# Kernel tuning notes

Measured on AMD Instinct MI355X. Metric: run time of the kernel, lower is better.

Reference implementation:

```python
import jax, jax.numpy as jnp
import numpy as np

N, R, C_IN, C_OUT, MODES = 8, 256, 64, 64, 16


def setup_inputs() -> dict:
    key = jax.random.key(0)
    k1, k2, k3, k4, k5 = jax.random.split(key, 5)
    # xavier-like scale used in the torch init: gain/(in*out)*sqrt(in+out) folded into std
    std = (1.0 / (C_IN * C_OUT)) * np.sqrt(2.0)  # small, keeps spectra sane
    return {
        "X": jax.random.normal(k1, (N, R, R, C_IN), dtype=jnp.float32),
        "W_res": jax.random.normal(k2, (C_IN, C_OUT), dtype=jnp.float32) / np.sqrt(C_IN),
        "b_res": jax.random.normal(k3, (C_OUT,), dtype=jnp.float32) * 0.01,
        "fw0": jax.random.normal(k4, (C_IN, C_OUT, MODES, MODES, 2), dtype=jnp.float32) * std,
        "fw1": jax.random.normal(k5, (C_IN, C_OUT, MODES, MODES, 2), dtype=jnp.float32) * std,
    }


def reference(X, W_res, b_res, fw0, fw1):
    # X: [N, r, r, in_dim]
    n, r, _, _ = X.shape
    modes = fw0.shape[2]
    out_dim = fw0.shape[1]

    res = X @ W_res + b_res  # [N, r, r, out_dim]  (dropout p=0.0 -> identity)

    Xc = jnp.transpose(X, (0, 3, 1, 2))  # [N, in, r, r]
    X_ft = jnp.fft.rfft2(Xc, s=(r, r), norm="ortho")  # [N, in, r, r//2+1] complex

    w0 = fw0[..., 0] + 1j * fw0[..., 1]  # [in, out, m, m] complex
    w1 = fw1[..., 0] + 1j * fw1[..., 1]

    top = jnp.einsum("bixy,ioxy->boxy", X_ft[:, :, :modes, :modes], w0)
    bot = jnp.einsum("bixy,ioxy->boxy", X_ft[:, :, r - modes :, :modes], w1)

    out_ft = jnp.zeros((n, out_dim, r, r // 2 + 1), dtype=X_ft.dtype)
    out_ft = out_ft.at[:, :, :modes, :modes].set(top)
    out_ft = out_ft.at[:, :, r - modes :, :modes].set(bot)

    Xo = jnp.fft.irfft2(out_ft, s=(r, r), norm="ortho")  # [N, out, r, r] real
    Xo = jnp.transpose(Xo, (0, 2, 3, 1))  # [N, r, r, out]
    return jax.nn.silu(Xo + res)
```

## Files before the change

kernel.cpp:

```cpp
#include <hip/hip_runtime.h>
#include <math.h>

#define RDIM 256
#define CIN 64
#define COUT 64
#define MODES 16
#define NB 8

typedef short short8 __attribute__((ext_vector_type(8)));
typedef float f32x4 __attribute__((ext_vector_type(4)));

__device__ __forceinline__ unsigned short f2b(float f) {
    unsigned u = __builtin_bit_cast(unsigned, f);
    unsigned r = (u + 0x7FFFu + ((u >> 16) & 1u)) >> 16;
    return (unsigned short)r;
}

__device__ __forceinline__ void build_tab(float2* tab) {
    for (int p = (int)threadIdx.x; p < 256; p += (int)blockDim.x) {
        float ang = (float)p * (float)(2.0 * M_PI / 256.0);
        float s, c;
        sincosf(ang, &s, &c);
        tab[p] = make_float2(c, s);
    }
}

__global__ __launch_bounds__(256) void k_tf(unsigned short* __restrict__ Tf) {
    int e = blockIdx.x * 256 + (int)threadIdx.x;
    int kyc = e >> 8, y = e & 255, ky = kyc >> 1;
    int p = (ky * y) & 255;
    float ang = (float)p * (float)(2.0 * M_PI / 256.0);
    float s, c;
    sincosf(ang, &s, &c);
    Tf[e] = f2b((kyc & 1) ? -s : c);
}

__global__ __launch_bounds__(256) void k_wt(const float* __restrict__ fw0,
                                            const float* __restrict__ fw1,
                                            float2* __restrict__ WT) {
    __shared__ float2 Ls[16][257];
    int blk = blockIdx.x;
    int arr = blk >> 8;
    int tile = blk & 255;
    const float2* s2 = (const float2*)(arr ? fw1 : fw0);
    int t = (int)threadIdx.x;
    for (int e = t; e < 4096; e += 256) {
        int oo = e >> 8;
        int q = e & 255;
        Ls[oo][q] = s2[(size_t)(tile * 16 + oo) * 256 + q];
    }
    __syncthreads();
    int i = (tile * 16) >> 6;
    int o0 = (tile * 16) & 63;
    for (int e = t; e < 4096; e += 256) {
        int oo = e & 15;
        int q = e >> 4;
        int mx = q >> 4, ky = q & 15;
        int m = arr * 16 + mx;
        WT[((size_t)(m * 16 + ky) * 64 + i) * 64 + o0 + oo] = Ls[oo][q];
    }
}

__global__ __launch_bounds__(256) void k_prep(const float* __restrict__ Wres,
                                              unsigned short* __restrict__ WbT,
                                              unsigned short* __restrict__ Tg) {
    int e = blockIdx.x * 256 + (int)threadIdx.x;
    if (e < 4096) {
        int o = e >> 6, k = e & 63;
        WbT[o * 64 + k] = f2b(Wres[k * 64 + o]);
    } else {
        int f = e - 4096;
        int y = f >> 5, kk = f & 31, ky = kk >> 1;
        int p = (ky * y) & 255;
        float ang = (float)p * (float)(2.0 * M_PI / 256.0);
        float s, c;
        sincosf(ang, &s, &c);
        Tg[f] = f2b((kk & 1) ? -s : c);
    }
}

__global__ __launch_bounds__(256) void k_fwd_y(const float* __restrict__ X,
                                               const unsigned short* __restrict__ Tf,
                                               float2* __restrict__ A) {
    __shared__ short8 Xb[64 * 32];
    int b = blockIdx.x >> 8;
    int x = blockIdx.x & 255;
    int t = (int)threadIdx.x;
    int w = t >> 6;
    int l = t & 63;

    const float* Xr = X + ((size_t)(b * 256 + x)) * 256 * 64;
#pragma unroll
    for (int s = 0; s < 8; s++) {
        int y8 = w * 8 + s;
        const float* base = Xr + (size_t)y8 * 512 + l;
        short8 hb;
#pragma unroll
        for (int j = 0; j < 8; j++) hb[j] = (short)f2b(base[j * 64]);
        Xb[l * 32 + (y8 ^ (l & 7))] = hb;
    }
    __syncthreads();

    int m16 = l & 15;
    int quad = l >> 4;
    int iRow = w * 16 + m16;
    int isw = iRow & 7;

    f32x4 acc0 = (f32x4){0.f, 0.f, 0.f, 0.f};
    f32x4 acc1 = (f32x4){0.f, 0.f, 0.f, 0.f};
    const unsigned short* T0 = Tf + (size_t)m16 * 256 + quad * 8;
#pragma unroll
    for (int ks = 0; ks < 8; ks++) {
        short8 a0 = *(const short8*)(T0 + ks * 32);
        short8 a1 = *(const short8*)(T0 + 4096 + ks * 32);
        int y8r = ks * 4 + quad;
        short8 bfrag = Xb[iRow * 32 + (y8r ^ isw)];
        acc0 = __builtin_amdgcn_mfma_f32_16x16x32_bf16(a0, bfrag, acc0, 0, 0, 0);
        acc1 = __builtin_amdgcn_mfma_f32_16x16x32_bf16(a1, bfrag, acc1, 0, 0, 0);
    }

    float2* Aout = A + ((size_t)(b * 256 + x)) * 16 * 64;
    int ky0 = (quad * 4) >> 1;
    Aout[(size_t)ky0 * 64 + iRow] = make_float2(acc0[0], acc0[1]);
    Aout[(size_t)(ky0 + 1) * 64 + iRow] = make_float2(acc0[2], acc0[3]);
    int ky1 = (16 + quad * 4) >> 1;
    Aout[(size_t)ky1 * 64 + iRow] = make_float2(acc1[0], acc1[1]);
    Aout[(size_t)(ky1 + 1) * 64 + iRow] = make_float2(acc1[2], acc1[3]);
}

__global__ __launch_bounds__(256) void k_fwd_x(const float2* __restrict__ A,
                                               float2* __restrict__ C) {
    __shared__ float2 tab[256];
    __shared__ float2 red[4 * 8 * 64];
    int bi = blockIdx.x;
    int b = bi >> 6;
    int ky = (bi >> 2) & 15;
    int mg = bi & 3;
    build_tab(tab);
    __syncthreads();
    int t = (int)threadIdx.x;
    int i = t & 63;
    int xg = t >> 6;
    float cr[8], ci[8];
    int pj[8], st[8];
#pragma unroll
    for (int j = 0; j < 8; j++) {
        cr[j] = 0.f; ci[j] = 0.f;
        int m = mg * 8 + j;
        int kx = (m < 16) ? m : (m + 224);
        pj[j] = (kx * xg) & 255;
        st[j] = (kx * 4) & 255;
    }
    const float2* Ap = A + ((size_t)b * 256) * 16 * 64 + ky * 64 + i;
    for (int x = xg; x < 256; x += 4) {
        float2 a = Ap[(size_t)x * 16 * 64];
#pragma unroll
        for (int j = 0; j < 8; j++) {
            float2 tc = tab[pj[j]];
            pj[j] = (pj[j] + st[j]) & 255;
            cr[j] += a.x * tc.x + a.y * tc.y;
            ci[j] += a.y * tc.x - a.x * tc.y;
        }
    }
#pragma unroll
    for (int j = 0; j < 8; j++) red[(xg * 8 + j) * 64 + i] = make_float2(cr[j], ci[j]);
    __syncthreads();
    const float sc = 1.0f / 256.0f;
    for (int e = t; e < 8 * 64; e += 256) {
        int j = e >> 6;
        int ii = e & 63;
        float2 s = red[j * 64 + ii];
        float2 s1 = red[(8 + j) * 64 + ii];
        float2 s2 = red[(16 + j) * 64 + ii];
        float2 s3 = red[(24 + j) * 64 + ii];
        float rr = (s.x + s1.x) + (s2.x + s3.x);
        float im = (s.y + s1.y) + (s2.y + s3.y);
        int m = mg * 8 + j;
        C[(((size_t)b * 16 + ky) * 32 + m) * 64 + ii] = make_float2(rr * sc, im * sc);
    }
}

__global__ __launch_bounds__(256) void k_mix(const float2* __restrict__ C,
                                             const float2* __restrict__ WT,
                                             float2* __restrict__ D) {
    __shared__ float2 Ws[64 * 64];
    __shared__ float2 Cs[8 * 64];
    __shared__ float2 red[4 * 8 * 64];
    int bi = blockIdx.x;
    int ky = bi >> 5;
    int m = bi & 31;
    int t = (int)threadIdx.x;
    const float4* Wsrc = (const float4*)(WT + ((size_t)(m * 16 + ky)) * 4096);
    float4* Wd = (float4*)Ws;
    for (int e = t; e < 2048; e += 256) Wd[e] = Wsrc[e];
    for (int e = t; e < 512; e += 256) {
        int b = e >> 6;
        int i = e & 63;
        Cs[e] = C[(((size_t)b * 16 + ky) * 32 + m) * 64 + i];
    }
    __syncthreads();
    int o = t & 63;
    int ig = t >> 6;
    float dr[8], di[8];
#pragma unroll
    for (int b = 0; b < 8; b++) { dr[b] = 0.f; di[b] = 0.f; }
    for (int i2 = ig * 16; i2 < ig * 16 + 16; i2++) {
        float2 w = Ws[i2 * 64 + o];
#pragma unroll
        for (int b = 0; b < 8; b++) {
            float2 c = Cs[b * 64 + i2];
            dr[b] += c.x * w.x - c.y * w.y;
            di[b] += c.x * w.y + c.y * w.x;
        }
    }
#pragma unroll
    for (int b = 0; b < 8; b++) red[(ig * 8 + b) * 64 + o] = make_float2(dr[b], di[b]);
    __syncthreads();
    for (int e = t; e < 512; e += 256) {
        int b = e >> 6;
        int oo = e & 63;
        float2 s = red[b * 64 + oo];
        float2 s1 = red[(8 + b) * 64 + oo];
        float2 s2 = red[(16 + b) * 64 + oo];
        float2 s3 = red[(24 + b) * 64 + oo];
        D[(((size_t)b * 16 + ky) * 32 + m) * 64 + oo] =
            make_float2((s.x + s1.x) + (s2.x + s3.x), (s.y + s1.y) + (s2.y + s3.y));
    }
}

__global__ __launch_bounds__(256) void k_inv_x(const float2* __restrict__ D,
                                               float2* __restrict__ G) {
    __shared__ float2 tab[256];
    __shared__ float2 Ds[32 * 64];
    int bi = blockIdx.x;
    int b = bi >> 7;
    int ky = (bi >> 3) & 15;
    int xc = bi & 7;
    build_tab(tab);
    int t = (int)threadIdx.x;
    const float4* Dsrc = (const float4*)(D + (((size_t)b * 16 + ky) * 32) * 64);
    float4* Dd = (float4*)Ds;
    for (int e = t; e < 1024; e += 256) Dd[e] = Dsrc[e];
    __syncthreads();
    int o = t & 63;
    int xg = t >> 6;
#pragma unroll
    for (int j = 0; j < 8; j++) {
        int x = xc * 32 + xg * 8 + j;
        int ex = (224 * x) & 255;
        float gr = 0.f, gi = 0.f;
        int p = 0;
#pragma unroll
        for (int m = 0; m < 32; m++) {
            float2 tc = tab[p];
            p = (p + x) & 255;
            if (m == 15) p = (p + ex) & 255;
            float2 d = Ds[m * 64 + o];
            gr += d.x * tc.x - d.y * tc.y;
            gi += d.x * tc.y + d.y * tc.x;
        }
        G[((size_t)(b * 256 + x) * 16 + ky) * 64 + o] = make_float2(gr, gi);
    }
}

__global__ __launch_bounds__(256) void k_out(const float* __restrict__ X,
                                             const float2* __restrict__ G,
                                             const unsigned short* __restrict__ WbT,
                                             const unsigned short* __restrict__ Tg,
                                             const float* __restrict__ bres,
                                             float* __restrict__ out) {
    __shared__ unsigned short Bsp[64 * 32];
    int b = blockIdx.x >> 8;
    int x = blockIdx.x & 255;
    int t = (int)threadIdx.x;

    const float2* Gp = G + ((size_t)(b * 256 + x)) * 16 * 64;
    for (int e = t; e < 1024; e += 256) {
        int ky = e >> 6, o = e & 63;
        float2 g = Gp[e];
        float sc = (ky == 0) ? (1.0f / 256.0f) : (2.0f / 256.0f);
        Bsp[o * 32 + 2 * ky]     = f2b(g.x * sc);
        Bsp[o * 32 + 2 * ky + 1] = f2b(g.y * sc);
    }
    __syncthreads();

    int w = t >> 6;
    int l = t & 63;
    int m16 = l & 15;
    int quad = l >> 4;

    short8 bw0[4], bw1[4], bs[4];
    float br[4];
#pragma unroll
    for (int nt = 0; nt < 4; nt++) {
        int o = nt * 16 + m16;
        bw0[nt] = *(const short8*)(WbT + o * 64 + quad * 8);
        bw1[nt] = *(const short8*)(WbT + o * 64 + 32 + quad * 8);
        bs[nt]  = *(const short8*)(Bsp + o * 32 + quad * 8);
        br[nt]  = bres[o];
    }

    const float* Xrow = X + ((size_t)(b * 256 + x)) * 256 * 64;
    float* orow = out + ((size_t)(b * 256 + x)) * 256 * 64;

    f32x4 acc[4][4];
#pragma unroll
    for (int mt = 0; mt < 4; mt++)
#pragma unroll
        for (int nt = 0; nt < 4; nt++) acc[mt][nt] = (f32x4){0.f, 0.f, 0.f, 0.f};

#pragma unroll
    for (int mt = 0; mt < 4; mt++) {
        int y = w * 64 + mt * 16 + m16;
        const float4* xp = (const float4*)(Xrow + (size_t)y * 64 + quad * 8);
        float4 v0 = xp[0], v1 = xp[1];
        const float4* xq = (const float4*)(Xrow + (size_t)y * 64 + 32 + quad * 8);
        float4 v2 = xq[0], v3 = xq[1];
        short8 a0, a1;
        a0[0] = (short)f2b(v0.x); a0[1] = (short)f2b(v0.y);
        a0[2] = (short)f2b(v0.z); a0[3] = (short)f2b(v0.w);
        a0[4] = (short)f2b(v1.x); a0[5] = (short)f2b(v1.y);
        a0[6] = (short)f2b(v1.z); a0[7] = (short)f2b(v1.w);
        a1[0] = (short)f2b(v2.x); a1[1] = (short)f2b(v2.y);
        a1[2] = (short)f2b(v2.z); a1[3] = (short)f2b(v2.w);
        a1[4] = (short)f2b(v3.x); a1[5] = (short)f2b(v3.y);
        a1[6] = (short)f2b(v3.z); a1[7] = (short)f2b(v3.w);
        short8 aT = *(const short8*)(Tg + (size_t)y * 32 + quad * 8);
#pragma unroll
        for (int nt = 0; nt < 4; nt++) {
            acc[mt][nt] = __builtin_amdgcn_mfma_f32_16x16x32_bf16(a0, bw0[nt], acc[mt][nt], 0, 0, 0);
            acc[mt][nt] = __builtin_amdgcn_mfma_f32_16x16x32_bf16(a1, bw1[nt], acc[mt][nt], 0, 0, 0);
            acc[mt][nt] = __builtin_amdgcn_mfma_f32_16x16x32_bf16(aT, bs[nt],  acc[mt][nt], 0, 0, 0);
        }
    }

#pragma unroll
    for (int mt = 0; mt < 4; mt++) {
#pragma unroll
        for (int nt = 0; nt < 4; nt++) {
            int o = nt * 16 + m16;
#pragma unroll
            for (int r = 0; r < 4; r++) {
                int y = w * 64 + mt * 16 + quad * 4 + r;
                float v = acc[mt][nt][r] + br[nt];
                float sg = __builtin_amdgcn_rcpf(1.0f + __expf(-v));
                orow[(size_t)y * 64 + o] = v * sg;
            }
        }
    }
}

extern "C" void kernel_launch(void* const* d_in, const int* in_sizes, int n_in,
                              void* d_out, int out_size, void* d_ws, size_t ws_size,
                              hipStream_t stream) {
    const float* X    = (const float*)d_in[0];
    const float* Wres = (const float*)d_in[1];
    const float* bres = (const float*)d_in[2];
    const float* fw0  = (const float*)d_in[3];
    const float* fw1  = (const float*)d_in[4];
    float* out = (float*)d_out;

    float2* A  = (float2*)d_ws;
    float2* C  = A + 2097152;
    float2* D  = C + 262144;
    float2* WT = D + 262144;
    float2* G  = A;
    unsigned short* WbT = (unsigned short*)C;
    unsigned short* Tg  = WbT + 4096;
    unsigned short* Tf  = (unsigned short*)D;

    k_wt<<<512, 256, 0, stream>>>(fw0, fw1, WT);
    k_tf<<<32, 256, 0, stream>>>(Tf);
    k_fwd_y<<<NB * 256, 256, 0, stream>>>(X, Tf, A);
    k_fwd_x<<<NB * 16 * 4, 256, 0, stream>>>(A, C);
    k_mix<<<16 * 32, 256, 0, stream>>>(C, WT, D);
    k_prep<<<48, 256, 0, stream>>>(Wres, WbT, Tg);
    k_inv_x<<<NB * 16 * 8, 256, 0, stream>>>(D, G);
    k_out<<<NB * 256, 256, 0, stream>>>(X, G, WbT, Tg, bres, out);
}
```

Baseline: 371.8 us.

## Move x-direction DFT stages onto bf16 MFMA and vectorize X loads

Replaces the scalar twiddle-table loops in the forward and inverse x-direction DFTs with bf16 MFMA matrix products against precomputed DFT matrices. The matrices are generated in k_tf and k_prep. The intermediate A layout is changed to [b,ky,x,i] so the forward x stage can read it contiguously, and the forward y stage now loads X as float4. This is meant to cut the FP32 ALU and LDS-lookup cost of the two DFT stages, at the price of bf16 rounding of intermediate spectra and extra table-generation work.

```diff
diff --git a/kernel.cpp b/kernel.cpp
--- a/kernel.cpp
+++ b/kernel.cpp
@@ -16,23 +16,36 @@
     return (unsigned short)r;
 }
 
-__device__ __forceinline__ void build_tab(float2* tab) {
-    for (int p = (int)threadIdx.x; p < 256; p += (int)blockDim.x) {
+__global__ __launch_bounds__(256) void k_tf(unsigned short* __restrict__ Tf2,
+                                            unsigned short* __restrict__ T2) {
+    int e = blockIdx.x * 256 + (int)threadIdx.x;
+    if (e < 8192) {
+        int kyc = e >> 8, k = e & 255;
+        int S = k >> 3, j = k & 7;
+        int w = S >> 3, h = (S >> 2) & 1, q = S & 3;
+        int y = w * 64 + q + 4 * (h * 8 + j);
+        int ky = kyc >> 1;
+        int p = (ky * y) & 255;
         float ang = (float)p * (float)(2.0 * M_PI / 256.0);
-        float s, c;
-        sincosf(ang, &s, &c);
-        tab[p] = make_float2(c, s);
-    }
-}
-
-__global__ __launch_bounds__(256) void k_tf(unsigned short* __restrict__ Tf) {
-    int e = blockIdx.x * 256 + (int)threadIdx.x;
-    int kyc = e >> 8, y = e & 255, ky = kyc >> 1;
-    int p = (ky * y) & 255;
-    float ang = (float)p * (float)(2.0 * M_PI / 256.0);
-    float s, c;
-    sincosf(ang, &s, &c);
-    Tf[e] = f2b((kyc & 1) ? -s : c);
+        float sz, cz;
+        sincosf(ang, &sz, &cz);
+        Tf2[e] = f2b((kyc & 1) ? -sz : cz);
+    } else {
+        int f = e - 8192;
+        int r = f >> 9, k = f & 511;
+        int S = k >> 3, j = k & 7;
+        int w = S >> 4, bp = (S >> 3) & 1, a = S & 7;
+        int d = j >> 1, c = j & 1;
+        int x = w * 64 + bp + 8 * a + 2 * d;
+        int m = r >> 1, cc = r & 1;
+        int kx = (m < 16) ? m : (m + 224);
+        int p = (kx * x) & 255;
+        float ang = (float)p * (float)(2.0 * M_PI / 256.0);
+        float sz, cz;
+        sincosf(ang, &sz, &cz);
+        float val = (cc == 0) ? (c ? sz : cz) : (c ? cz : -sz);
+        T2[f] = f2b(val * (1.0f / 256.0f));
+    }
 }
 
 __global__ __launch_bounds__(256) void k_wt(const float* __restrict__ fw0,
@@ -63,19 +76,32 @@
 
 __global__ __launch_bounds__(256) void k_prep(const float* __restrict__ Wres,
                                               unsigned short* __restrict__ WbT,
-                                              unsigned short* __restrict__ Tg) {
+                                              unsigned short* __restrict__ Tg,
+                                              unsigned short* __restrict__ A2) {
     int e = blockIdx.x * 256 + (int)threadIdx.x;
     if (e < 4096) {
         int o = e >> 6, k = e & 63;
         WbT[o * 64 + k] = f2b(Wres[k * 64 + o]);
-    } else {
+    } else if (e < 12288) {
         int f = e - 4096;
         int y = f >> 5, kk = f & 31, ky = kk >> 1;
         int p = (ky * y) & 255;
         float ang = (float)p * (float)(2.0 * M_PI / 256.0);
-        float s, c;
-        sincosf(ang, &s, &c);
-        Tg[f] = f2b((kk & 1) ? -s : c);
+        float sz, cz;
+        sincosf(ang, &sz, &cz);
+        Tg[f] = f2b((kk & 1) ? -sz : cz);
+    } else {
+        int f = e - 12288;
+        int comp = f >> 14, g = f & 16383;
+        int x = g >> 6, k = g & 63;
+        int m = k >> 1, c = k & 1;
+        int kx = (m < 16) ? m : (m + 224);
+        int p = (kx * x) & 255;
+        float ang = (float)p * (float)(2.0 * M_PI / 256.0);
+        float sz, cz;
+        sincosf(ang, &sz, &cz);
+        float val = (comp == 0) ? (c ? -sz : cz) : (c ? cz : sz);
+        A2[f] = f2b(val);
     }
 }
 
@@ -88,16 +114,29 @@
     int t = (int)threadIdx.x;
     int w = t >> 6;
     int l = t & 63;
-
-    const float* Xr = X + ((size_t)(b * 256 + x)) * 256 * 64;
-#pragma unroll
-    for (int s = 0; s < 8; s++) {
-        int y8 = w * 8 + s;
-        const float* base = Xr + (size_t)y8 * 512 + l;
-        short8 hb;
-#pragma unroll
-        for (int j = 0; j < 8; j++) hb[j] = (short)f2b(base[j * 64]);
-        Xb[l * 32 + (y8 ^ (l & 7))] = hb;
+    int q = l >> 4;
+    int f4 = l & 15;
+    int i0 = f4 * 4;
+
+    const float4* X4 = (const float4*)(X + ((size_t)(b * 256 + x)) * 256 * 64);
+#pragma unroll
+    for (int h = 0; h < 2; h++) {
+        float4 v[8];
+#pragma unroll
+        for (int n = 0; n < 8; n++) {
+            int y = w * 64 + q + 4 * (h * 8 + n);
+            v[n] = X4[y * 16 + f4];
+        }
+        const float* vf = (const float*)v;
+        int s = w * 8 + h * 4 + q;
+#pragma unroll
+        for (int di = 0; di < 4; di++) {
+            int i = i0 + di;
+            short8 hb;
+#pragma unroll
+            for (int j = 0; j < 8; j++) hb[j] = (short)f2b(vf[j * 4 + di]);
+            Xb[i * 32 + (s ^ (i & 7))] = hb;
+        }
     }
     __syncthreads();
 
@@ -113,70 +152,77 @@
     for (int ks = 0; ks < 8; ks++) {
         short8 a0 = *(const short8*)(T0 + ks * 32);
         short8 a1 = *(const short8*)(T0 + 4096 + ks * 32);
-        int y8r = ks * 4 + quad;
-        short8 bfrag = Xb[iRow * 32 + (y8r ^ isw)];
+        short8 bfrag = Xb[iRow * 32 + ((ks * 4 + quad) ^ isw)];
         acc0 = __builtin_amdgcn_mfma_f32_16x16x32_bf16(a0, bfrag, acc0, 0, 0, 0);
         acc1 = __builtin_amdgcn_mfma_f32_16x16x32_bf16(a1, bfrag, acc1, 0, 0, 0);
     }
 
-    float2* Aout = A + ((size_t)(b * 256 + x)) * 16 * 64;
-    int ky0 = (quad * 4) >> 1;
-    Aout[(size_t)ky0 * 64 + iRow] = make_float2(acc0[0], acc0[1]);
-    Aout[(size_t)(ky0 + 1) * 64 + iRow] = make_float2(acc0[2], acc0[3]);
-    int ky1 = (16 + quad * 4) >> 1;
-    Aout[(size_t)ky1 * 64 + iRow] = make_float2(acc1[0], acc1[1]);
-    Aout[(size_t)(ky1 + 1) * 64 + iRow] = make_float2(acc1[2], acc1[3]);
+    float2* Ab = A + ((size_t)(b * 16) * 256 + x) * 64;
+    int ky0 = quad * 2;
+    Ab[(size_t)(ky0)     * 16384 + iRow] = make_float2(acc0[0], acc0[1]);
+    Ab[(size_t)(ky0 + 1) * 16384 + iRow] = make_float2(acc0[2], acc0[3]);
+    Ab[(size_t)(ky0 + 8) * 16384 + iRow] = make_float2(acc1[0], acc1[1]);
+    Ab[(size_t)(ky0 + 9) * 16384 + iRow] = make_float2(acc1[2], acc1[3]);
 }
 
 __global__ __launch_bounds__(256) void k_fwd_x(const float2* __restrict__ A,
+                                               const unsigned short* __restrict__ T2,
                                                float2* __restrict__ C) {
-    __shared__ float2 tab[256];
-    __shared__ float2 red[4 * 8 * 64];
+    __shared__ short8 Bs[64 * 64];
     int bi = blockIdx.x;
-    int b = bi >> 6;
-    int ky = (bi >> 2) & 15;
-    int mg = bi & 3;
-    build_tab(tab);
-    __syncthreads();
-    int t = (int)threadIdx.x;
-    int i = t & 63;
-    int xg = t >> 6;
-    float cr[8], ci[8];
-    int pj[8], st[8];
-#pragma unroll
-    for (int j = 0; j < 8; j++) {
-        cr[j] = 0.f; ci[j] = 0.f;
-        int m = mg * 8 + j;
-        int kx = (m < 16) ? m : (m + 224);
-        pj[j] = (kx * xg) & 255;
-        st[j] = (kx * 4) & 255;
-    }
-    const float2* Ap = A + ((size_t)b * 256) * 16 * 64 + ky * 64 + i;
-    for (int x = xg; x < 256; x += 4) {
-        float2 a = Ap[(size_t)x * 16 * 64];
-#pragma unroll
-        for (int j = 0; j < 8; j++) {
-            float2 tc = tab[pj[j]];
-            pj[j] = (pj[j] + st[j]) & 255;
-            cr[j] += a.x * tc.x + a.y * tc.y;
-            ci[j] += a.y * tc.x - a.x * tc.y;
-        }
-    }
-#pragma unroll
-    for (int j = 0; j < 8; j++) red[(xg * 8 + j) * 64 + i] = make_float2(cr[j], ci[j]);
-    __syncthreads();
-    const float sc = 1.0f / 256.0f;
-    for (int e = t; e < 8 * 64; e += 256) {
-        int j = e >> 6;
-        int ii = e & 63;
-        float2 s = red[j * 64 + ii];
-        float2 s1 = red[(8 + j) * 64 + ii];
-        float2 s2 = red[(16 + j) * 64 + ii];
-        float2 s3 = red[(24 + j) * 64 + ii];
-        float rr = (s.x + s1.x) + (s2.x + s3.x);
-        float im = (s.y + s1.y) + (s2.y + s3.y);
-        int m = mg * 8 + j;
-        C[(((size_t)b * 16 + ky) * 32 + m) * 64 + ii] = make_float2(rr * sc, im * sc);
+    int b = bi >> 4;
+    int ky = bi & 15;
+    int t = (int)threadIdx.x;
+    int w = t >> 6, l = t & 63;
+    int i2 = (l & 31) * 2;
+    int bp = l >> 5;
+    const float4* A4 = (const float4*)(A + ((size_t)(b * 16 + ky)) * 256 * 64);
+#pragma unroll
+    for (int a = 0; a < 8; a++) {
+        float4 v[4];
+#pragma unroll
+        for (int d4 = 0; d4 < 4; d4++) {
+            int xx = w * 64 + bp + 8 * a + 2 * d4;
+            v[d4] = A4[xx * 32 + (l & 31)];
+        }
+        int S = w * 16 + bp * 8 + a;
+        short8 h0, h1;
+        h0[0] = (short)f2b(v[0].x); h0[1] = (short)f2b(v[0].y);
+        h0[2] = (short)f2b(v[1].x); h0[3] = (short)f2b(v[1].y);
+        h0[4] = (short)f2b(v[2].x); h0[5] = (short)f2b(v[2].y);
+        h0[6] = (short)f2b(v[3].x); h0[7] = (short)f2b(v[3].y);
+        h1[0] = (short)f2b(v[0].z); h1[1] = (short)f2b(v[0].w);
+        h1[2] = (short)f2b(v[1].z); h1[3] = (short)f2b(v[1].w);
+        h1[4] = (short)f2b(v[2].z); h1[5] = (short)f2b(v[2].w);
+        h1[6] = (short)f2b(v[3].z); h1[7] = (short)f2b(v[3].w);
+        Bs[i2 * 64 + (S ^ (i2 & 7))] = h0;
+        Bs[(i2 + 1) * 64 + (S ^ ((i2 + 1) & 7))] = h1;
+    }
+    __syncthreads();
+
+    int m16 = l & 15, quad = l >> 4;
+    int iRow = w * 16 + m16;
+    int isw = iRow & 7;
+    f32x4 acc[4];
+#pragma unroll
+    for (int mt = 0; mt < 4; mt++) acc[mt] = (f32x4){0.f, 0.f, 0.f, 0.f};
+    const unsigned short* Tp = T2 + (size_t)m16 * 512 + quad * 8;
+#pragma unroll
+    for (int ks = 0; ks < 16; ks++) {
+        short8 bfrag = Bs[iRow * 64 + ((ks * 4 + quad) ^ isw)];
+#pragma unroll
+        for (int mt = 0; mt < 4; mt++) {
+            short8 af = *(const short8*)(Tp + mt * 8192 + ks * 32);
+            acc[mt] = __builtin_amdgcn_mfma_f32_16x16x32_bf16(af, bfrag, acc[mt], 0, 0, 0);
+        }
+    }
+
+    float2* Cb = C + ((size_t)(b * 16 + ky)) * 32 * 64;
+#pragma unroll
+    for (int mt = 0; mt < 4; mt++) {
+        int m0 = mt * 8 + quad * 2;
+        Cb[(size_t)m0 * 64 + iRow]       = make_float2(acc[mt][0], acc[mt][1]);
+        Cb[(size_t)(m0 + 1) * 64 + iRow] = make_float2(acc[mt][2], acc[mt][3]);
     }
 }
 
@@ -229,38 +275,76 @@
 }
 
 __global__ __launch_bounds__(256) void k_inv_x(const float2* __restrict__ D,
+                                               const unsigned short* __restrict__ A2,
                                                float2* __restrict__ G) {
-    __shared__ float2 tab[256];
-    __shared__ float2 Ds[32 * 64];
+    __shared__ short8 Bd[64 * 8];
     int bi = blockIdx.x;
-    int b = bi >> 7;
-    int ky = (bi >> 3) & 15;
-    int xc = bi & 7;
-    build_tab(tab);
-    int t = (int)threadIdx.x;
-    const float4* Dsrc = (const float4*)(D + (((size_t)b * 16 + ky) * 32) * 64);
-    float4* Dd = (float4*)Ds;
-    for (int e = t; e < 1024; e += 256) Dd[e] = Dsrc[e];
-    __syncthreads();
-    int o = t & 63;
-    int xg = t >> 6;
-#pragma unroll
-    for (int j = 0; j < 8; j++) {
-        int x = xc * 32 + xg * 8 + j;
-        int ex = (224 * x) & 255;
-        float gr = 0.f, gi = 0.f;
-        int p = 0;
-#pragma unroll
-        for (int m = 0; m < 32; m++) {
-            float2 tc = tab[p];
-            p = (p + x) & 255;
-            if (m == 15) p = (p + ex) & 255;
-            float2 d = Ds[m * 64 + o];
-            gr += d.x * tc.x - d.y * tc.y;
-            gi += d.x * tc.y + d.y * tc.x;
-        }
-        G[((size_t)(b * 256 + x) * 16 + ky) * 64 + o] = make_float2(gr, gi);
-    }
+    int b = bi >> 5;
+    int ky = (bi >> 1) & 15;
+    int xh = bi & 1;
+    int t = (int)threadIdx.x;
+    int w = t >> 6, l = t & 63;
+    const float2* Dp = D + ((size_t)(b * 16 + ky)) * 32 * 64;
+    float2 dv[8];
+#pragma unroll
+    for (int s = 0; s < 8; s++) dv[s] = Dp[(size_t)(w * 8 + s) * 64 + l];
+    short8 h0, h1;
+    h0[0] = (short)f2b(dv[0].x); h0[1] = (short)f2b(dv[0].y);
+    h0[2] = (short)f2b(dv[1].x); h0[3] = (short)f2b(dv[1].y);
+    h0[4] = (short)f2b(dv[2].x); h0[5] = (short)f2b(dv[2].y);
+    h0[6] = (short)f2b(dv[3].x); h0[7] = (short)f2b(dv[3].y);
+    h1[0] = (short)f2b(dv[4].x); h1[1] = (short)f2b(dv[4].y);
+    h1[2] = (short)f2b(dv[5].x); h1[3] = (short)f2b(dv[5].y);
+    h1[4] = (short)f2b(dv[6].x); h1[5] = (short)f2b(dv[6].y);
+    h1[6] = (short)f2b(dv[7].x); h1[7] = (short)f2b(dv[7].y);
+    int sl = l & 7;
+    Bd[l * 8 + ((2 * w) ^ sl)]     = h0;
+    Bd[l * 8 + ((2 * w + 1) ^ sl)] = h1;
+    __syncthreads();
+
+    int m16 = l & 15, quad = l >> 4;
+    int x0 = xh * 128 + w * 32;
+    f32x4 acc[2][4][2];
+#pragma unroll
+    for (int mt = 0; mt < 2; mt++)
+#pragma unroll
+        for (int nt = 0; nt < 4; nt++)
+#pragma unroll
+            for (int c = 0; c < 2; c++) acc[mt][nt][c] = (f32x4){0.f, 0.f, 0.f, 0.f};
+
+#pragma unroll
+    for (int ks = 0; ks < 2; ks++) {
+        short8 ar[2], ai[2];
+#pragma unroll
+        for (int mt = 0; mt < 2; mt++) {
+            int xr = x0 + mt * 16 + m16;
+            ar[mt] = *(const short8*)(A2 + (size_t)xr * 64 + ks * 32 + quad * 8);
+            ai[mt] = *(const short8*)(A2 + 16384 + (size_t)xr * 64 + ks * 32 + quad * 8);
+        }
+#pragma unroll
+        for (int nt = 0; nt < 4; nt++) {
+            int o = nt * 16 + m16;
+            short8 bf = Bd[o * 8 + ((ks * 4 + quad) ^ (o & 7))];
+#pragma unroll
+            for (int mt = 0; mt < 2; mt++) {
+                acc[mt][nt][0] = __builtin_amdgcn_mfma_f32_16x16x32_bf16(ar[mt], bf, acc[mt][nt][0], 0, 0, 0);
+                acc[mt][nt][1] = __builtin_amdgcn_mfma_f32_16x16x32_bf16(ai[mt], bf, acc[mt][nt][1], 0, 0, 0);
+            }
+        }
+    }
+
+#pragma unroll
+    for (int mt = 0; mt < 2; mt++)
+#pragma unroll
+        for (int nt = 0; nt < 4; nt++) {
+            int o = nt * 16 + m16;
+#pragma unroll
+            for (int r = 0; r < 4; r++) {
+                int x = x0 + mt * 16 + quad * 4 + r;
+                G[((size_t)(b * 256 + x) * 16 + ky) * 64 + o] =
+                    make_float2(acc[mt][nt][0][r], acc[mt][nt][1][r]);
+            }
+        }
 }
 
 __global__ __launch_bounds__(256) void k_out(const float* __restrict__ X,
@@ -365,16 +449,18 @@
     float2* D  = C + 262144;
     float2* WT = D + 262144;
     float2* G  = A;
+    unsigned short* Tf2 = (unsigned short*)D;
+    unsigned short* T2  = Tf2 + 8192;
     unsigned short* WbT = (unsigned short*)C;
     unsigned short* Tg  = WbT + 4096;
-    unsigned short* Tf  = (unsigned short*)D;
+    unsigned short* A2  = Tg + 8192;
 
     k_wt<<<512, 256, 0, stream>>>(fw0, fw1, WT);
-    k_tf<<<32, 256, 0, stream>>>(Tf);
-    k_fwd_y<<<NB * 256, 256, 0, stream>>>(X, Tf, A);
-    k_fwd_x<<<NB * 16 * 4, 256, 0, stream>>>(A, C);
+    k_tf<<<160, 256, 0, stream>>>(Tf2, T2);
+    k_fwd_y<<<NB * 256, 256, 0, stream>>>(X, Tf2, A);
+    k_fwd_x<<<128, 256, 0, stream>>>(A, T2, C);
     k_mix<<<16 * 32, 256, 0, stream>>>(C, WT, D);
-    k_prep<<<48, 256, 0, stream>>>(Wres, WbT, Tg);
-    k_inv_x<<<NB * 16 * 8, 256, 0, stream>>>(D, G);
+    k_prep<<<176, 256, 0, stream>>>(Wres, WbT, Tg, A2);
+    k_inv_x<<<256, 256, 0, stream>>>(D, A2, G);
     k_out<<<NB * 256, 256, 0, stream>>>(X, G, WbT, Tg, bres, out);
 }
```

Result: faster. 324.6 us (-12.7%).
